# Kernel optimization log

Hardware: AMD Instinct MI355X
Metric: run time of the kernel (lower is better)

The kernel has to match this reference:

```python
import jax, jax.numpy as jnp
import numpy as np

N, NFEAT, NHID, NCLASS, E = 100000, 128, 128, 40, 1600000

def _glorot(key, fan_in, fan_out):
    lim = float(np.sqrt(6.0 / (fan_in + fan_out)))
    return jax.random.uniform(key, (fan_in, fan_out), jnp.float32, -lim, lim)

def setup_inputs() -> dict:
    key = jax.random.key(0)
    ks = jax.random.split(key, 20)
    inp = {
        'x': jax.random.normal(ks[0], (N, NFEAT), jnp.float32),
        'edge_index': jax.random.randint(ks[1], (2, E), 0, N, jnp.int64 if jax.config.x64_enabled else jnp.int32),
    }
    dims = [(NFEAT, NHID), (NHID, NHID), (NHID, NHID), (NHID, NHID), (NHID, NHID), (NHID, NHID)]
    names = ['gc1_w1', 'gc1_w2', 'gc2_w1', 'gc2_w2', 'gc3_w1', 'gc3_w2']
    for i, (nm, (fi, fo)) in enumerate(zip(names, dims)):
        inp[nm] = _glorot(ks[2 + i], fi, fo)
        inp[nm.replace('w', 'b')] = jnp.zeros((fo,), jnp.float32)
    inp['lin1_w'] = _glorot(ks[10], 3 * NHID, 3 * NHID)
    inp['lin1_b'] = jnp.zeros((3 * NHID,), jnp.float32)
    inp['lin2_w'] = _glorot(ks[11], 3 * NHID, NCLASS)
    inp['lin2_b'] = jnp.zeros((NCLASS,), jnp.float32)
    return inp

def _gin_conv(x, src, dst, w1, b1, w2, b2):
    # GINConv, eps=0: mlp(x + sum_{j->i} x_j)
    agg = jax.ops.segment_sum(x[src], dst, num_segments=N)  # [N, d]
    h = jax.nn.relu((x + agg) @ w1 + b1)
    return jax.nn.relu(h @ w2 + b2)

def reference(x, edge_index, gc1_w1, gc1_b1, gc1_w2, gc1_b2,
              gc2_w1, gc2_b1, gc2_w2, gc2_b2,
              gc3_w1, gc3_b1, gc3_w2, gc3_b2,
              lin1_w, lin1_b, lin2_w, lin2_b):
    src, dst = edge_index[0], edge_index[1]
    h1 = _gin_conv(x, src, dst, gc1_w1, gc1_b1, gc1_w2, gc1_b2)
    h2 = _gin_conv(h1, src, dst, gc2_w1, gc2_b1, gc2_w2, gc2_b2)
    h3 = _gin_conv(h2, src, dst, gc3_w1, gc3_b1, gc3_w2, gc3_b2)
    h = jnp.concatenate([h1, h2, h3], axis=1)  # [N, 3*nhid]
    h = jax.nn.relu(h @ lin1_w + lin1_b)  # dropout inactive in eval mode
    h = h @ lin2_w + lin2_b
    return jax.nn.log_softmax(h, axis=1)
```

## Files before the change

kernel.cpp:

```cpp
#include <hip/hip_runtime.h>

#define N_NODES 100000
#define NEDGE   1600000
#define NHID    128
#define NCLASS  40

#define AGG_NODES 128
#define COLV_LDS  3072
#define FILL_RANGE  12500
#define WPREP_TOT   264192
#define EPB 2048
#define NBB 782
#define C2B 128

using bf16x8 = __attribute__((ext_vector_type(8))) short;
using f32x4  = __attribute__((ext_vector_type(4))) float;

__device__ __forceinline__ float bf2f(unsigned short s) {
    unsigned u = ((unsigned)s) << 16; float f; __builtin_memcpy(&f, &u, 4); return f;
}
__device__ __forceinline__ unsigned short f2bf(float f) {
    unsigned u; __builtin_memcpy(&u, &f, 4);
    u = u + 0x7fffu + ((u >> 16) & 1u);
    return (unsigned short)(u >> 16);
}

__device__ __forceinline__ void gld16(const void* g, void* l) {
    __builtin_amdgcn_global_load_lds(g, l, 16, 0, 0);
}

__global__ __launch_bounds__(256) void k_bucket(const int* __restrict__ ei,
                                                unsigned* __restrict__ pairs,
                                                int* __restrict__ bofs, int* __restrict__ bcnt) {
    __shared__ int wcnt[4][8];
    __shared__ int wbase[4][8];
    __shared__ int sbase[9];
    const int tid = threadIdx.x, lane = tid & 63, w = tid >> 6;
    const int e0 = blockIdx.x * EPB;
    const unsigned long long below = (1ull << lane) - 1ull;

    int dl[8], src[8], sl[8], posw[8];
    int cnt[8] = {0, 0, 0, 0, 0, 0, 0, 0};
    #pragma unroll
    for (int k = 0; k < 8; ++k) {
        int e = e0 + w * 512 + k * 64 + lane;
        bool v = e < NEDGE;
        int d = v ? ei[NEDGE + e] : -1;
        src[k] = v ? ei[e] : 0;
        int slc = v ? d / FILL_RANGE : -1;
        sl[k] = slc;
        dl[k] = v ? d - slc * FILL_RANGE : 0;
        posw[k] = 0;
        #pragma unroll
        for (int s = 0; s < 8; ++s) {
            unsigned long long mask = __ballot(slc == s);
            if (slc == s) posw[k] = cnt[s] + (int)__popcll(mask & below);
            cnt[s] += (int)__popcll(mask);
        }
    }
    if (lane == 0) {
        #pragma unroll
        for (int s = 0; s < 8; ++s) wcnt[w][s] = cnt[s];
    }
    __syncthreads();
    if (tid == 0) {
        int run = 0;
        for (int s = 0; s < 8; ++s) {
            sbase[s] = run;
            for (int w2 = 0; w2 < 4; ++w2) { wbase[w2][s] = run; run += wcnt[w2][s]; }
        }
        sbase[8] = run;
        for (int s = 0; s < 8; ++s) {
            bofs[blockIdx.x * 8 + s] = e0 + sbase[s];
            bcnt[blockIdx.x * 8 + s] = sbase[s + 1] - sbase[s];
        }
    }
    __syncthreads();
    #pragma unroll
    for (int k = 0; k < 8; ++k) {
        if (sl[k] >= 0)
            pairs[e0 + wbase[w][sl[k]] + posw[k]] = ((unsigned)dl[k] << 17) | (unsigned)src[k];
    }
}

__global__ __launch_bounds__(256) void k_count2(const unsigned* __restrict__ pairs,
                                                const int* __restrict__ bofs,
                                                const int* __restrict__ bcnt,
                                                int* __restrict__ cnt) {
    int s = blockIdx.x & 7, bb0 = blockIdx.x >> 3;
    int lo = s * FILL_RANGE;
    for (int bb = bb0; bb < NBB; bb += C2B) {
        int beg = bofs[bb * 8 + s], n = bcnt[bb * 8 + s];
        for (int i = threadIdx.x; i < n; i += 256)
            atomicAdd(&cnt[lo + (int)(pairs[beg + i] >> 17)], 1);
    }
}

__global__ void k_scan1(const int* __restrict__ cnt, int* __restrict__ rp, int* __restrict__ bsum) {
    __shared__ int sh[256];
    int t = threadIdx.x, base = blockIdx.x * 1024;
    int v[4]; int s = 0;
    for (int k = 0; k < 4; ++k) { int i = base + t * 4 + k; v[k] = (i < N_NODES) ? cnt[i] : 0; s += v[k]; }
    sh[t] = s; __syncthreads();
    for (int off = 1; off < 256; off <<= 1) {
        int x = (t >= off) ? sh[t - off] : 0;
        __syncthreads();
        sh[t] += x;
        __syncthreads();
    }
    int excl = sh[t] - s;
    for (int k = 0; k < 4; ++k) { int i = base + t * 4 + k; if (i < N_NODES) rp[i] = excl; excl += v[k]; }
    if (t == 255) bsum[blockIdx.x] = sh[255];
}

__global__ void k_scan2(int* __restrict__ bsum, int nb) {
    __shared__ int sh[256];
    int t = threadIdx.x;
    int v = (t < nb) ? bsum[t] : 0;
    sh[t] = v; __syncthreads();
    for (int off = 1; off < 256; off <<= 1) {
        int x = (t >= off) ? sh[t - off] : 0;
        __syncthreads();
        sh[t] += x;
        __syncthreads();
    }
    if (t < nb) bsum[t] = sh[t] - v;
}

__global__ void k_scan3(int* __restrict__ rp, const int* __restrict__ bsum, int* __restrict__ cur) {
    int base = blockIdx.x * 1024;
    int off = bsum[blockIdx.x];
    for (int k = 0; k < 4; ++k) {
        int i = base + threadIdx.x * 4 + k;
        if (i < N_NODES) { int v = rp[i] + off; rp[i] = v; cur[i] = v; }
    }
    if (blockIdx.x == 0 && threadIdx.x == 0) rp[N_NODES] = NEDGE;
}

__global__ __launch_bounds__(256) void k_fill2(const unsigned* __restrict__ pairs,
                                               const int* __restrict__ bofs,
                                               const int* __restrict__ bcnt,
                                               int* __restrict__ cur, int* __restrict__ colv) {
    int s = blockIdx.x & 7, bb0 = blockIdx.x >> 3;
    int lo = s * FILL_RANGE;
    for (int bb = bb0; bb < NBB; bb += C2B) {
        int beg = bofs[bb * 8 + s], n = bcnt[bb * 8 + s];
        for (int i = threadIdx.x; i < n; i += 256) {
            unsigned p = pairs[beg + i];
            int d = lo + (int)(p >> 17);
            int q = atomicAdd(&cur[d], 1);
            colv[q] = (int)(p & 0x1FFFFu);
        }
    }
}

__global__ void k_wprep_all(const float* __restrict__ g0, const float* __restrict__ g1,
                            const float* __restrict__ g2, const float* __restrict__ g3,
                            const float* __restrict__ g4, const float* __restrict__ g5,
                            const float* __restrict__ l1w, const float* __restrict__ l2w,
                            unsigned short* __restrict__ dst) {
    int idx = blockIdx.x * 256 + threadIdx.x;
    if (idx >= WPREP_TOT) return;
    const float* w; int local, K, O;
    if (idx < 98304) {
        int r = idx >> 14; local = idx & 16383; K = 128; O = 128;
        w = r == 0 ? g0 : r == 1 ? g1 : r == 2 ? g2 : r == 3 ? g3 : r == 4 ? g4 : g5;
    } else if (idx < 245760) {
        local = idx - 98304; K = 384; O = 384; w = l1w;
    } else {
        local = idx - 245760; K = 384; O = 40; w = l2w;
    }
    int kss = K >> 5;
    int e = local & 7, lane = (local >> 3) & 63, rest = local >> 9;
    int ks = rest % kss, ot = rest / kss;
    int c = ot * 16 + (lane & 15);
    int k = ks * 32 + (lane >> 4) * 8 + e;
    float v = (c < O) ? w[k * O + c] : 0.f;
    dst[idx] = f2bf(v);
}

__global__ void k_xprep(const float* __restrict__ x, unsigned short* __restrict__ xs) {
    int s = blockIdx.x & 3;
    int rest = (blockIdx.x >> 2) * 256 + threadIdx.x;
    if (rest >= N_NODES * 16) return;
    int n = rest >> 4, wrd = rest & 15;
    float2 v = *(const float2*)(x + (size_t)n * 128 + s * 32 + wrd * 2);
    ((unsigned*)xs)[(size_t)s * N_NODES * 16 + rest] =
        (unsigned)f2bf(v.x) | ((unsigned)f2bf(v.y) << 16);
}

__device__ __forceinline__ void acc8(float* acc, uint4 f, float m) {
    unsigned u[4] = {f.x, f.y, f.z, f.w};
    for (int d = 0; d < 4; ++d) {
        acc[2 * d]     = fmaf(m, bf2f((unsigned short)u[d]), acc[2 * d]);
        acc[2 * d + 1] = fmaf(m, bf2f((unsigned short)(u[d] >> 16)), acc[2 * d + 1]);
    }
}

__global__ __launch_bounds__(512) void k_aggs(const unsigned short* __restrict__ feat,
                                              unsigned short* __restrict__ tout,
                                              const int* __restrict__ rp,
                                              const int* __restrict__ colv) {
    __shared__ int scol[COLV_LDS + 8];
    __shared__ int srp[AGG_NODES + 1];
    const int s = blockIdx.x & 3;
    const int chunk = blockIdx.x >> 2;
    const int tid = threadIdx.x;
    const int nbase = chunk * AGG_NODES;

    for (int i = tid; i <= AGG_NODES; i += 512) {
        int n = nbase + i;
        srp[i] = rp[n <= N_NODES ? n : N_NODES];
    }
    __syncthreads();
    const int ebase = srp[0];
    const int ecount = srp[AGG_NODES] - ebase;
    const int elds = ecount < COLV_LDS ? ecount : COLV_LDS;
    for (int i = tid; i < elds; i += 512) scol[i] = colv[ebase + i];
    if (tid < 8) scol[elds + tid] = 0;
    __syncthreads();

    const unsigned* fs = (const unsigned*)feat + (size_t)s * N_NODES * 16;
    unsigned* ts = (unsigned*)tout + (size_t)s * N_NODES * 16;

    const int sub = tid >> 2, q = tid & 3;
    const int node = nbase + sub;
    if (node >= N_NODES) return;
    const int off = q * 4;
    const int e0 = srp[sub] - ebase, e1 = srp[sub + 1] - ebase;

    float acc[8];
    {
        uint4 a = *(const uint4*)(fs + (size_t)node * 16 + off);
        unsigned u[4] = {a.x, a.y, a.z, a.w};
        for (int d = 0; d < 4; ++d) {
            acc[2 * d]     = bf2f((unsigned short)u[d]);
            acc[2 * d + 1] = bf2f((unsigned short)(u[d] >> 16));
        }
    }

    if (ecount <= COLV_LDS) {
        int e = e0;
        const int efull = e0 + ((e1 - e0) & ~7);
        for (; e < efull; e += 8) {
            int j[8];
            #pragma unroll
            for (int k = 0; k < 8; ++k) j[k] = scol[e + k];
            uint4 f[8];
            #pragma unroll
            for (int k = 0; k < 8; ++k)
                f[k] = *(const uint4*)(fs + (size_t)j[k] * 16 + off);
            #pragma unroll
            for (int k = 0; k < 8; ++k) acc8(acc, f[k], 1.f);
        }
        if (e < e1) {
            int j[8]; float m[8];
            #pragma unroll
            for (int k = 0; k < 8; ++k) {
                int ee = e + k;
                bool v = ee < e1;
                j[k] = v ? scol[ee] : node;
                m[k] = v ? 1.f : 0.f;
            }
            uint4 f[8];
            #pragma unroll
            for (int k = 0; k < 8; ++k)
                f[k] = *(const uint4*)(fs + (size_t)j[k] * 16 + off);
            #pragma unroll
            for (int k = 0; k < 8; ++k) acc8(acc, f[k], m[k]);
        }
    } else {
        for (int e = e0; e < e1; e += 8) {
            int j[8]; float m[8];
            #pragma unroll
            for (int k = 0; k < 8; ++k) {
                int ee = e + k;
                bool v = ee < e1;
                int idx = ee < COLV_LDS ? scol[ee] : colv[ebase + ee];
                j[k] = v ? idx : node;
                m[k] = v ? 1.f : 0.f;
            }
            uint4 f[8];
            #pragma unroll
            for (int k = 0; k < 8; ++k)
                f[k] = *(const uint4*)(fs + (size_t)j[k] * 16 + off);
            #pragma unroll
            for (int k = 0; k < 8; ++k) acc8(acc, f[k], m[k]);
        }
    }

    uint4 o;
    o.x = (unsigned)f2bf(acc[0]) | ((unsigned)f2bf(acc[1]) << 16);
    o.y = (unsigned)f2bf(acc[2]) | ((unsigned)f2bf(acc[3]) << 16);
    o.z = (unsigned)f2bf(acc[4]) | ((unsigned)f2bf(acc[5]) << 16);
    o.w = (unsigned)f2bf(acc[6]) | ((unsigned)f2bf(acc[7]) << 16);
    *(uint4*)(ts + (size_t)node * 16 + off) = o;
}

__global__ __launch_bounds__(512) void k_mlp(
    const unsigned short* __restrict__ tin,
    const unsigned short* __restrict__ w1t, const float* __restrict__ b1,
    const unsigned short* __restrict__ w2t, const float* __restrict__ b2,
    unsigned short* __restrict__ hout) {
    __shared__ __align__(16) char tlds[4 * 8192];
    __shared__ __align__(16) char hlds[4 * 8192];
    const int tid = threadIdx.x, lane = tid & 63, w = tid >> 6;
    const int l15 = lane & 15, lg = lane >> 4;
    const int nbase = blockIdx.x * 128;
    const int rx = (l15 >> 1) & 3;

    #pragma unroll
    for (int i = 0; i < 4; ++i) {
        int c = w + i * 8;
        int s = c >> 3, rblk = c & 7;
        int node = nbase + rblk * 16 + (lane >> 2);
        if (node >= N_NODES) node = 0;
        int hsrc = (lane & 3) ^ ((lane >> 3) & 3);
        gld16(tin + ((size_t)s * N_NODES + node) * 32 + hsrc * 8,
              tlds + c * 1024);
    }

    bf16x8 B1[4], B2[4];
    const int col = w * 16 + l15;
    const float bias1 = b1[col], bias2 = b2[col];
    #pragma unroll
    for (int ks = 0; ks < 4; ++ks) {
        B1[ks] = *(const bf16x8*)(w1t + ((size_t)(w * 4 + ks) * 64 + lane) * 8);
        B2[ks] = *(const bf16x8*)(w2t + ((size_t)(w * 4 + ks) * 64 + lane) * 8);
    }
    __syncthreads();

    {
        const int hoff = ((lg ^ rx) << 4);
        bf16x8 A[2][4];
        #pragma unroll
        for (int ks = 0; ks < 4; ++ks)
            A[0][ks] = *(const bf16x8*)(tlds + ks * 8192 + l15 * 64 + hoff);
        #pragma unroll
        for (int m = 0; m < 8; ++m) {
            int cur = m & 1, nxt = cur ^ 1;
            if (m < 7) {
                int row = (m + 1) * 16 + l15;
                #pragma unroll
                for (int ks = 0; ks < 4; ++ks)
                    A[nxt][ks] = *(const bf16x8*)(tlds + ks * 8192 + row * 64 + hoff);
            }
            f32x4 acc = {0.f, 0.f, 0.f, 0.f};
            #pragma unroll
            for (int ks = 0; ks < 4; ++ks)
                acc = __builtin_amdgcn_mfma_f32_16x16x32_bf16(A[cur][ks], B1[ks], acc, 0, 0, 0);
            #pragma unroll
            for (int r = 0; r < 4; ++r) {
                int row = m * 16 + lg * 4 + r;
                int rw = (2 * lg + (r >> 1)) & 3;
                int h = (w & 1) * 2 + (l15 >> 3);
                float v = acc[r] + bias1; v = v > 0.f ? v : 0.f;
                *(unsigned short*)(hlds + (w >> 1) * 8192 + row * 64 +
                                   ((h ^ rw) << 4) + (l15 & 7) * 2) = f2bf(v);
            }
        }
    }
    __syncthreads();

    {
        const int hoff = ((lg ^ rx) << 4);
        bf16x8 A[2][4];
        #pragma unroll
        for (int ks = 0; ks < 4; ++ks)
            A[0][ks] = *(const bf16x8*)(hlds + ks * 8192 + l15 * 64 + hoff);
        #pragma unroll
        for (int m = 0; m < 8; ++m) {
            int cur = m & 1, nxt = cur ^ 1;
            if (m < 7) {
                int row = (m + 1) * 16 + l15;
                #pragma unroll
                for (int ks = 0; ks < 4; ++ks)
                    A[nxt][ks] = *(const bf16x8*)(hlds + ks * 8192 + row * 64 + hoff);
            }
            f32x4 acc = {0.f, 0.f, 0.f, 0.f};
            #pragma unroll
            for (int ks = 0; ks < 4; ++ks)
                acc = __builtin_amdgcn_mfma_f32_16x16x32_bf16(A[cur][ks], B2[ks], acc, 0, 0, 0);
            #pragma unroll
            for (int r = 0; r < 4; ++r) {
                int node = nbase + m * 16 + lg * 4 + r;
                if (node < N_NODES) {
                    float v = acc[r] + bias2; v = v > 0.f ? v : 0.f;
                    hout[((size_t)(w >> 1) * N_NODES + node) * 32 + (w & 1) * 16 + l15] = f2bf(v);
                }
            }
        }
    }
}

__global__ __launch_bounds__(512, 4) void k_final(
    const unsigned short* __restrict__ h1, const unsigned short* __restrict__ h2,
    const unsigned short* __restrict__ h3,
    const unsigned short* __restrict__ l1t, const float* __restrict__ l1b,
    const unsigned short* __restrict__ l2t, const float* __restrict__ l2b,
    float* __restrict__ out) {
    __shared__ __align__(16) char lds[12 * 4096];
    const int tid = threadIdx.x, lane = tid & 63, w = tid >> 6;
    const int l15 = lane & 15, lg = lane >> 4;
    const int nbase = blockIdx.x * 64;
    const int rx = (l15 >> 1) & 3;

    #pragma unroll
    for (int i = 0; i < 6; ++i) {
        int c = w + i * 8;
        int g = c >> 2, rblk = c & 3;
        int part = g >> 2, slice = g & 3;
        int node = nbase + rblk * 16 + (lane >> 2);
        if (node >= N_NODES) node = 0;
        int hsrc = (lane & 3) ^ ((lane >> 3) & 3);
        const unsigned short* hp = part == 0 ? h1 : (part == 1 ? h2 : h3);
        gld16(hp + ((size_t)slice * N_NODES + node) * 32 + hsrc * 8,
              lds + c * 1024);
    }

    bf16x8 B[2][3];
    #pragma unroll
    for (int ot = 0; ot < 3; ++ot)
        B[0][ot] = *(const bf16x8*)(l1t + ((size_t)((w * 3 + ot) * 12) * 64 + lane) * 8);
    __syncthreads();

    f32x4 acc[4][3];
    #pragma unroll
    for (int m = 0; m < 4; ++m)
        #pragma unroll
        for (int ot = 0; ot < 3; ++ot) acc[m][ot] = {0.f, 0.f, 0.f, 0.f};
    {
        const int hoff = ((lg ^ rx) << 4);
        #pragma unroll
        for (int ks = 0; ks < 12; ++ks) {
            int cur = ks & 1, nxt = cur ^ 1;
            if (ks < 11) {
                #pragma unroll
                for (int ot = 0; ot < 3; ++ot)
                    B[nxt][ot] = *(const bf16x8*)(l1t + ((size_t)((w * 3 + ot) * 12 + ks + 1) * 64 + lane) * 8);
            }
            bf16x8 A[4];
            #pragma unroll
            for (int m = 0; m < 4; ++m) {
                int row = m * 16 + l15;
                A[m] = *(const bf16x8*)(lds + ks * 4096 + row * 64 + hoff);
            }
            #pragma unroll
            for (int ot = 0; ot < 3; ++ot)
                #pragma unroll
                for (int m = 0; m < 4; ++m)
                    acc[m][ot] = __builtin_amdgcn_mfma_f32_16x16x32_bf16(A[m], B[cur][ot], acc[m][ot], 0, 0, 0);
        }
    }
    __syncthreads();

    #pragma unroll
    for (int ot = 0; ot < 3; ++ot) {
        int c = (w * 3 + ot) * 16 + l15;
        int gc = c >> 5, h = (c >> 3) & 3, b2i = (c & 7) * 2;
        float bias = l1b[c];
        #pragma unroll
        for (int m = 0; m < 4; ++m)
            #pragma unroll
            for (int r = 0; r < 4; ++r) {
                int row = m * 16 + lg * 4 + r;
                int rw = (2 * lg + (r >> 1)) & 3;
                float v = acc[m][ot][r] + bias; v = v > 0.f ? v : 0.f;
                *(unsigned short*)(lds + gc * 4096 + row * 64 + ((h ^ rw) << 4) + b2i) = f2bf(v);
            }
    }
    __syncthreads();

    if (w < 4) {
        f32x4 acc2[3];
        #pragma unroll
        for (int ot = 0; ot < 3; ++ot) acc2[ot] = {0.f, 0.f, 0.f, 0.f};
        {
            const int row = w * 16 + l15;
            const int hoff = ((lg ^ rx) << 4);
            bf16x8 C2[2][3];
            #pragma unroll
            for (int ot = 0; ot < 3; ++ot)
                C2[0][ot] = *(const bf16x8*)(l2t + ((size_t)(ot * 12) * 64 + lane) * 8);
            #pragma unroll
            for (int ks = 0; ks < 12; ++ks) {
                int cur = ks & 1, nxt = cur ^ 1;
                if (ks < 11) {
                    #pragma unroll
                    for (int ot = 0; ot < 3; ++ot)
                        C2[nxt][ot] = *(const bf16x8*)(l2t + ((size_t)(ot * 12 + ks + 1) * 64 + lane) * 8);
                }
                bf16x8 A2 = *(const bf16x8*)(lds + ks * 4096 + row * 64 + hoff);
                #pragma unroll
                for (int ot = 0; ot < 3; ++ot)
                    acc2[ot] = __builtin_amdgcn_mfma_f32_16x16x32_bf16(A2, C2[cur][ot], acc2[ot], 0, 0, 0);
            }
        }

        int c0 = l15;
        #pragma unroll
        for (int r = 0; r < 4; ++r) {
            float v0 = acc2[0][r] + l2b[c0];
            float v1 = acc2[1][r] + l2b[c0 + 16];
            float v2 = (c0 < 8) ? (acc2[2][r] + l2b[c0 + 32]) : -1e30f;
            float mx = fmaxf(fmaxf(v0, v1), v2);
            for (int msk = 1; msk < 16; msk <<= 1) mx = fmaxf(mx, __shfl_xor(mx, msk));
            float s = __expf(v0 - mx) + __expf(v1 - mx) + ((c0 < 8) ? __expf(v2 - mx) : 0.f);
            for (int msk = 1; msk < 16; msk <<= 1) s += __shfl_xor(s, msk);
            float lse = mx + __logf(s);
            int node = nbase + w * 16 + lg * 4 + r;
            if (node < N_NODES) {
                out[(size_t)node * 40 + c0] = v0 - lse;
                out[(size_t)node * 40 + c0 + 16] = v1 - lse;
                if (c0 < 8) out[(size_t)node * 40 + c0 + 32] = v2 - lse;
            }
        }
    }
}

extern "C" void kernel_launch(void* const* d_in, const int* in_sizes, int n_in,
                              void* d_out, int out_size, void* d_ws, size_t ws_size,
                              hipStream_t stream) {
    const float* x  = (const float*)d_in[0];
    const int*   ei = (const int*)d_in[1];
    const float* gw1[3] = {(const float*)d_in[2],  (const float*)d_in[6],  (const float*)d_in[10]};
    const float* gb1[3] = {(const float*)d_in[3],  (const float*)d_in[7],  (const float*)d_in[11]};
    const float* gw2[3] = {(const float*)d_in[4],  (const float*)d_in[8],  (const float*)d_in[12]};
    const float* gb2[3] = {(const float*)d_in[5],  (const float*)d_in[9],  (const float*)d_in[13]};
    const float* l1w = (const float*)d_in[14];
    const float* l1b = (const float*)d_in[15];
    const float* l2w = (const float*)d_in[16];
    const float* l2b = (const float*)d_in[17];
    float* out = (float*)d_out;

    char* p = (char*)d_ws;
    auto alloc = [&](size_t bytes) { char* q = p; p += (bytes + 255) & ~(size_t)255; return q; };
    int* rp    = (int*)alloc(4 * (N_NODES + 1));
    int* cnt   = (int*)alloc(4 * N_NODES);
    int* cur   = (int*)alloc(4 * N_NODES);
    int* bsum  = (int*)alloc(4 * 256);
    int* bofs  = (int*)alloc(4 * NBB * 8);
    int* bcnt  = (int*)alloc(4 * NBB * 8);
    unsigned* pairs = (unsigned*)alloc(4 * (size_t)NEDGE);
    int* colv  = (int*)alloc(4 * (size_t)NEDGE);
    unsigned short* t  = (unsigned short*)alloc(2 * (size_t)N_NODES * 128);
    unsigned short* h1 = (unsigned short*)alloc(2 * (size_t)N_NODES * 128);
    unsigned short* h2 = (unsigned short*)alloc(2 * (size_t)N_NODES * 128);
    unsigned short* h3 = (unsigned short*)alloc(2 * (size_t)N_NODES * 128);
    unsigned short* xs = h3;
    unsigned short* wt[6];
    for (int i = 0; i < 6; ++i) wt[i] = (unsigned short*)alloc(2 * 128 * 128);
    unsigned short* l1t = (unsigned short*)alloc(2 * 384 * 384);
    unsigned short* l2t = (unsigned short*)alloc(2 * 48 * 384);

    const int nb = (N_NODES + 1023) / 1024;
    hipMemsetAsync(cnt, 0, 4 * N_NODES, stream);
    k_bucket<<<NBB, 256, 0, stream>>>(ei, pairs, bofs, bcnt);
    k_count2<<<8 * C2B, 256, 0, stream>>>(pairs, bofs, bcnt, cnt);
    k_scan1<<<nb, 256, 0, stream>>>(cnt, rp, bsum);
    k_scan2<<<1, 256, 0, stream>>>(bsum, nb);
    k_scan3<<<nb, 256, 0, stream>>>(rp, bsum, cur);
    k_fill2<<<8 * C2B, 256, 0, stream>>>(pairs, bofs, bcnt, cur, colv);

    k_wprep_all<<<(WPREP_TOT + 255) / 256, 256, 0, stream>>>(
        gw1[0], gw2[0], gw1[1], gw2[1], gw1[2], gw2[2], l1w, l2w, wt[0]);

    k_xprep<<<4 * ((N_NODES * 16 + 255) / 256), 256, 0, stream>>>(x, xs);

    const int gagg = ((N_NODES + AGG_NODES - 1) / AGG_NODES) * 4;
    const int gtile2 = (N_NODES + 127) / 128;
    const int gtile1 = (N_NODES + 63) / 64;
    k_aggs<<<gagg, 512, 0, stream>>>(xs, t, rp, colv);
    k_mlp<<<gtile2, 512, 0, stream>>>(t, wt[0], gb1[0], wt[1], gb2[0], h1);
    k_aggs<<<gagg, 512, 0, stream>>>(h1, t, rp, colv);
    k_mlp<<<gtile2, 512, 0, stream>>>(t, wt[2], gb1[1], wt[3], gb2[1], h2);
    k_aggs<<<gagg, 512, 0, stream>>>(h2, t, rp, colv);
    k_mlp<<<gtile2, 512, 0, stream>>>(t, wt[4], gb1[2], wt[5], gb2[2], h3);
    k_final<<<gtile1, 512, 0, stream>>>(h1, h2, h3, l1t, l1b, l2t, l2b, out);
}
```

Measured before the change: 482.8 us.

## Replace global atomics in CSR count/fill with per-block LDS node-range partitioning

```diff
diff --git a/kernel.cpp b/kernel.cpp
--- a/kernel.cpp
+++ b/kernel.cpp
@@ -11,7 +11,7 @@
 #define WPREP_TOT   264192
 #define EPB 2048
 #define NBB 782
-#define C2B 128
+#define SUBN 196
 
 using bf16x8 = __attribute__((ext_vector_type(8))) short;
 using f32x4  = __attribute__((ext_vector_type(4))) float;
@@ -83,17 +83,27 @@
     }
 }
 
-__global__ __launch_bounds__(256) void k_count2(const unsigned* __restrict__ pairs,
-                                                const int* __restrict__ bofs,
-                                                const int* __restrict__ bcnt,
-                                                int* __restrict__ cnt) {
-    int s = blockIdx.x & 7, bb0 = blockIdx.x >> 3;
-    int lo = s * FILL_RANGE;
-    for (int bb = bb0; bb < NBB; bb += C2B) {
+__global__ __launch_bounds__(256) void k_cnt3(const unsigned* __restrict__ pairs,
+                                              const int* __restrict__ bofs,
+                                              const int* __restrict__ bcnt,
+                                              int* __restrict__ cnt) {
+    __shared__ int lcnt[SUBN];
+    const int s = blockIdx.x & 7, sub = blockIdx.x >> 3;
+    const int nlo = sub * SUBN;
+    const int nhi = (nlo + SUBN < FILL_RANGE) ? nlo + SUBN : FILL_RANGE;
+    const int tid = threadIdx.x;
+    for (int i = tid; i < SUBN; i += 256) lcnt[i] = 0;
+    __syncthreads();
+    for (int bb = 0; bb < NBB; ++bb) {
         int beg = bofs[bb * 8 + s], n = bcnt[bb * 8 + s];
-        for (int i = threadIdx.x; i < n; i += 256)
-            atomicAdd(&cnt[lo + (int)(pairs[beg + i] >> 17)], 1);
-    }
+        for (int i = tid; i < n; i += 256) {
+            int dl = (int)(pairs[beg + i] >> 17);
+            if (dl >= nlo && dl < nhi) atomicAdd(&lcnt[dl - nlo], 1);
+        }
+    }
+    __syncthreads();
+    int base = s * FILL_RANGE + nlo;
+    for (int i = tid; i < nhi - nlo; i += 256) cnt[base + i] = lcnt[i];
 }
 
 __global__ void k_scan1(const int* __restrict__ cnt, int* __restrict__ rp, int* __restrict__ bsum) {
@@ -127,29 +137,43 @@
     if (t < nb) bsum[t] = sh[t] - v;
 }
 
-__global__ void k_scan3(int* __restrict__ rp, const int* __restrict__ bsum, int* __restrict__ cur) {
+__global__ void k_scan3(int* __restrict__ rp, const int* __restrict__ bsum) {
     int base = blockIdx.x * 1024;
     int off = bsum[blockIdx.x];
     for (int k = 0; k < 4; ++k) {
         int i = base + threadIdx.x * 4 + k;
-        if (i < N_NODES) { int v = rp[i] + off; rp[i] = v; cur[i] = v; }
+        if (i < N_NODES) rp[i] += off;
     }
     if (blockIdx.x == 0 && threadIdx.x == 0) rp[N_NODES] = NEDGE;
 }
 
-__global__ __launch_bounds__(256) void k_fill2(const unsigned* __restrict__ pairs,
+__global__ __launch_bounds__(256) void k_fill3(const unsigned* __restrict__ pairs,
                                                const int* __restrict__ bofs,
                                                const int* __restrict__ bcnt,
-                                               int* __restrict__ cur, int* __restrict__ colv) {
-    int s = blockIdx.x & 7, bb0 = blockIdx.x >> 3;
-    int lo = s * FILL_RANGE;
-    for (int bb = bb0; bb < NBB; bb += C2B) {
+                                               const int* __restrict__ rp,
+                                               int* __restrict__ colv) {
+    __shared__ int lcur[SUBN];
+    __shared__ int lrp[SUBN];
+    const int s = blockIdx.x & 7, sub = blockIdx.x >> 3;
+    const int nlo = sub * SUBN;
+    const int nhi = (nlo + SUBN < FILL_RANGE) ? nlo + SUBN : FILL_RANGE;
+    const int tid = threadIdx.x;
+    const int gbase = s * FILL_RANGE + nlo;
+    for (int i = tid; i < SUBN; i += 256) {
+        lcur[i] = 0;
+        lrp[i] = (gbase + i <= N_NODES) ? rp[gbase + i] : 0;
+    }
+    __syncthreads();
+    for (int bb = 0; bb < NBB; ++bb) {
         int beg = bofs[bb * 8 + s], n = bcnt[bb * 8 + s];
-        for (int i = threadIdx.x; i < n; i += 256) {
+        for (int i = tid; i < n; i += 256) {
             unsigned p = pairs[beg + i];
-            int d = lo + (int)(p >> 17);
-            int q = atomicAdd(&cur[d], 1);
-            colv[q] = (int)(p & 0x1FFFFu);
+            int dl = (int)(p >> 17);
+            if (dl >= nlo && dl < nhi) {
+                int li = dl - nlo;
+                int pos = atomicAdd(&lcur[li], 1);
+                colv[lrp[li] + pos] = (int)(p & 0x1FFFFu);
+            }
         }
     }
 }
@@ -537,7 +561,6 @@
     auto alloc = [&](size_t bytes) { char* q = p; p += (bytes + 255) & ~(size_t)255; return q; };
     int* rp    = (int*)alloc(4 * (N_NODES + 1));
     int* cnt   = (int*)alloc(4 * N_NODES);
-    int* cur   = (int*)alloc(4 * N_NODES);
     int* bsum  = (int*)alloc(4 * 256);
     int* bofs  = (int*)alloc(4 * NBB * 8);
     int* bcnt  = (int*)alloc(4 * NBB * 8);
@@ -554,13 +577,12 @@
     unsigned short* l2t = (unsigned short*)alloc(2 * 48 * 384);
 
     const int nb = (N_NODES + 1023) / 1024;
-    hipMemsetAsync(cnt, 0, 4 * N_NODES, stream);
     k_bucket<<<NBB, 256, 0, stream>>>(ei, pairs, bofs, bcnt);
-    k_count2<<<8 * C2B, 256, 0, stream>>>(pairs, bofs, bcnt, cnt);
+    k_cnt3<<<8 * 64, 256, 0, stream>>>(pairs, bofs, bcnt, cnt);
     k_scan1<<<nb, 256, 0, stream>>>(cnt, rp, bsum);
     k_scan2<<<1, 256, 0, stream>>>(bsum, nb);
-    k_scan3<<<nb, 256, 0, stream>>>(rp, bsum, cur);
-    k_fill2<<<8 * C2B, 256, 0, stream>>>(pairs, bofs, bcnt, cur, colv);
+    k_scan3<<<nb, 256, 0, stream>>>(rp, bsum);
+    k_fill3<<<8 * 64, 256, 0, stream>>>(pairs, bofs, bcnt, rp, colv);
 
     k_wprep_all<<<(WPREP_TOT + 255) / 256, 256, 0, stream>>>(
         gw1[0], gw2[0], gw1[1], gw2[1], gw1[2], gw2[2], l1w, l2w, wt[0]);
```

Result: slower. 1.026 ms (+112.6%).
